# Optimization experiments

Measured on AMD Instinct MI355X. Metric: run time of the kernel, lower is better.

The kernel has to match this reference:

```python
import jax, jax.numpy as jnp
import numpy as np

ANGRES = 5  # u = v = angRes, n = 25


def _l2norm(x, axis):
    n = jnp.sqrt(jnp.sum(x * x, axis=axis, keepdims=True))
    return x / jnp.maximum(n, 1e-12)  # matches torch F.normalize eps


def _cos_attn(qm, km, vm):
    # qm: (b, M, K), km: (b, K, M), vm: (b, M, K)
    q = _l2norm(qm, -1)
    k = _l2norm(km, -2)
    att = jax.nn.softmax(q @ k, axis=-1)  # (b, M, M)
    return att @ vm


def _af_attn(x, u, v):  # AngularFrequencyAttention: b c (u v) h w -> b (c u) (h v w)
    b, c, n, h, w = x.shape
    t = x.reshape(b, c, u, v, h, w)
    qm = t.transpose(0, 1, 2, 4, 3, 5).reshape(b, c * u, h * v * w)   # (b,c,u,h,v,w)
    km = t.transpose(0, 4, 3, 5, 1, 2).reshape(b, h * v * w, c * u)   # (b,h,v,w,c,u)
    o = _cos_attn(qm, km, qm)
    o = o.reshape(b, c, u, h, v, w).transpose(0, 1, 2, 4, 3, 5).reshape(b, c, n, h, w)
    return o + x


def _sa_attn(x, u, v):  # SpatialAngularAttention: b c (u v) h w -> b (h u) (c v w)
    b, c, n, h, w = x.shape
    t = x.reshape(b, c, u, v, h, w)
    qm = t.transpose(0, 4, 2, 1, 3, 5).reshape(b, h * u, c * v * w)   # (b,h,u,c,v,w)
    km = t.transpose(0, 1, 3, 5, 4, 2).reshape(b, c * v * w, h * u)   # (b,c,v,w,h,u)
    o = _cos_attn(qm, km, qm)
    o = o.reshape(b, h, u, c, v, w).transpose(0, 3, 2, 4, 1, 5).reshape(b, c, n, h, w)
    return o + x


def _sf_attn(x, u, v):  # SpatialFrequencyAttention: b c (u v) h w -> b (c h) (w u v)
    b, c, n, h, w = x.shape
    t = x.reshape(b, c, u, v, h, w)
    qm = t.transpose(0, 1, 4, 5, 2, 3).reshape(b, c * h, w * u * v)   # (b,c,h,w,u,v)
    km = t.transpose(0, 5, 2, 3, 1, 4).reshape(b, w * u * v, c * h)   # (b,w,u,v,c,h)
    o = _cos_attn(qm, km, qm)
    o = o.reshape(b, c, h, w, u, v).transpose(0, 1, 4, 5, 2, 3).reshape(b, c, n, h, w)
    return o + x


def _layernorm(x, g, bta, eps=1e-5):
    mu = jnp.mean(x, -1, keepdims=True)
    var = jnp.mean(jnp.square(x - mu), -1, keepdims=True)
    return (x - mu) * jax.lax.rsqrt(var + eps) * g + bta


def setup_inputs() -> dict:
    key = jax.random.key(0)
    k0, k1, k2 = jax.random.split(key, 3)
    b, c, n, h, w = 4, 64, 25, 48, 48
    x = jax.random.normal(k0, (b, c, n, h, w), dtype=jnp.float32)
    gamma = jnp.ones((3 * c,), dtype=jnp.float32)
    beta = jnp.zeros((3 * c,), dtype=jnp.float32)
    w1 = jax.random.normal(k1, (3 * c, c), dtype=jnp.float32) * 0.02
    w2 = jax.random.normal(k2, (c, c), dtype=jnp.float32) * 0.02
    return {"x": x, "gamma": gamma, "beta": beta, "w1": w1, "w2": w2}


def reference(x, gamma, beta, w1, w2):
    u = v = ANGRES
    b, c, n, h, w = x.shape
    sf = _sf_attn(x, u, v)
    af = _af_attn(x, u, v)
    sa = _sa_attn(x, u, v)
    cat = jnp.concatenate([sf, af, sa], axis=1)            # (b, 3c, n, h, w)
    f = cat.transpose(0, 3, 4, 2, 1).reshape(b * h * w, n, 3 * c)
    y = _layernorm(f, gamma, beta)
    y = jax.nn.relu(y @ w1) @ w2                            # (bhw, n, c); dropout p=0.01 is eval-identity
    out = y.reshape(b, h, w, n, c).transpose(0, 4, 3, 1, 2) + x
    return out
```

## Files before the change

kernel.cpp:

```cpp
#include <hip/hip_runtime.h>
#include <stdint.h>

typedef __attribute__((ext_vector_type(8))) short bf16x8;
typedef __attribute__((ext_vector_type(4))) float f32x4;

__device__ __forceinline__ float b2f(short s) {
  union { unsigned u; float f; } a; a.u = ((unsigned)(unsigned short)s) << 16; return a.f;
}
__device__ __forceinline__ short f2b(float f) {
  union { float f; unsigned u; } a; a.f = f;
  unsigned r = a.u + 0x7fffu + ((a.u >> 16) & 1u);
  return (short)(r >> 16);
}
__device__ __forceinline__ void gload16(const void* g, void* l) {
  __builtin_amdgcn_global_load_lds((__attribute__((address_space(1))) void*)g,
                                   (__attribute__((address_space(3))) void*)l, 16, 0, 0);
}

#define SWZ(row, col) ((col) ^ (((row) & 7) << 3))

__global__ __launch_bounds__(256) void permute_sf_k(const float* __restrict__ x,
                                                    short* __restrict__ Q,
                                                    float* __restrict__ inv) {
  __shared__ float buf[4][1200];
  int wave = threadIdx.x >> 6, lane = threadIdx.x & 63;
  int gr = blockIdx.x * 4 + wave;
  int b = gr / 3072, m = gr - b * 3072;
  int c = m / 48, hh = m - c * 48;
  const float* xb = x + (long)(b * 64 + c) * 57600 + hh * 48;
  for (int uv = 0; uv < 25; ++uv)
    if (lane < 48) buf[wave][uv * 48 + lane] = xb[uv * 2304 + lane];
  __syncthreads();
  short* Qr = Q + (long)gr * 1280;
  float ss = 0.f;
  for (int k = lane; k < 1280; k += 64) {
    float v = 0.f;
    if (k < 1200) { int wv = k / 25, uv = k - wv * 25; v = buf[wave][uv * 48 + wv]; }
    ss += v * v;
    Qr[k] = f2b(v);
  }
  #pragma unroll
  for (int o = 32; o >= 1; o >>= 1) ss += __shfl_xor(ss, o, 64);
  if (lane == 0) inv[gr] = 1.0f / fmaxf(sqrtf(ss), 1e-12f);
}

__global__ __launch_bounds__(256) void permtr_all_k(const float* __restrict__ x,
    short* __restrict__ Qaf, short* __restrict__ QTaf,
    short* __restrict__ Qsa, short* __restrict__ QTsa,
    float* __restrict__ ssaf, float* __restrict__ sssa) {
  __shared__ short t[32][33];
  int bid = blockIdx.x;
  int isAF = (bid < 17280);
  int M, Mp, Kp, kt, mt, b;
  short *Q, *QT; float* ss;
  if (isAF) { M = 320; Mp = 384; Kp = 11520; kt = bid % 360; int r = bid / 360; mt = r % 12; b = r / 12;
              Q = Qaf; QT = QTaf; ss = ssaf; }
  else { int id = bid - 17280; M = 240; Mp = 256; Kp = 15360; kt = id % 480; int r = id / 480; mt = r % 8; b = r / 8;
         Q = Qsa; QT = QTsa; ss = sssa; }
  int k0 = kt * 32, m0 = mt * 32;
  int tx = threadIdx.x & 31, ty = threadIdx.x >> 5;
  const float* xb = x + (long)b * 3686400;
  #pragma unroll
  for (int i = 0; i < 32; i += 8) {
    int m = m0 + ty + i, k = k0 + tx;
    float v = 0.f;
    if (m < M) {
      int q1 = k / 240, r2 = k - q1 * 240;
      int v5 = r2 / 48, wv = r2 - v5 * 48;
      int a1 = m / 5, u = m - a1 * 5;
      long xi = isAF ? ((long)a1 * 25 + u * 5 + v5) * 2304 + q1 * 48 + wv
                     : ((long)q1 * 25 + u * 5 + v5) * 2304 + a1 * 48 + wv;
      v = xb[xi];
    }
    t[ty + i][tx] = f2b(v);
  }
  __syncthreads();
  long Qb = (long)b * Mp * Kp;
  #pragma unroll
  for (int i = 0; i < 32; i += 8)
    Q[Qb + (long)(m0 + ty + i) * Kp + k0 + tx] = t[ty + i][tx];
  #pragma unroll
  for (int i = 0; i < 32; i += 8)
    QT[Qb + (long)(k0 + ty + i) * Mp + m0 + tx] = t[tx][ty + i];
  if (threadIdx.x < 32 && m0 + (int)threadIdx.x < M) {
    float s = 0.f;
    #pragma unroll
    for (int k = 0; k < 32; ++k) { float f = b2f(t[threadIdx.x][k]); s += f * f; }
    atomicAdd(&ss[b * Mp + m0 + threadIdx.x], s);
  }
}

__global__ __launch_bounds__(256) void transpose_k(const short* __restrict__ in, short* __restrict__ out,
                                                   int R, int C) {
  __shared__ short t[32][33];
  long base = (long)blockIdx.z * R * C;
  int c0 = blockIdx.x * 32, r0 = blockIdx.y * 32;
  int tx = threadIdx.x & 31, ty = threadIdx.x >> 5;
  #pragma unroll
  for (int i = 0; i < 32; i += 8)
    t[ty + i][tx] = in[base + (long)(r0 + ty + i) * C + c0 + tx];
  __syncthreads();
  #pragma unroll
  for (int i = 0; i < 32; i += 8)
    out[base + (long)(c0 + ty + i) * R + r0 + tx] = t[tx][ty + i];
}

__global__ __launch_bounds__(256, 2) void gemm1_tri_k(const short* __restrict__ Q,
                                                      const float* __restrict__ invn,
                                                      short* __restrict__ att,
                                                      float* __restrict__ rowsum) {
  __shared__ short sm[32768];
  int tid = threadIdx.x, wave = tid >> 6, lane = tid & 63;
  int la = lane & 15, lb = lane >> 4;
  int bat = blockIdx.z;
  int bx = blockIdx.x, yt = 0, rem = bx;
  while (rem >= 24 - yt) { rem -= 24 - yt; ++yt; }
  int xt = yt + rem;
  const short* Qb = Q + (long)bat * 3932160L;
  const float* inv = invn + (long)bat * 3072;
  int row0 = yt * 128, col0 = xt * 128;
  f32x4 acc[4][4] = {};
  int wr = wave >> 1, wc = wave & 1;
  int rloc = tid >> 3, cbase = (tid & 7) * 8;
  int ldsoff = tid * 8;

  const short *pA[4], *pB[4];
  #pragma unroll
  for (int p = 0; p < 4; ++p) {
    int row = p * 32 + rloc;
    int sc = SWZ(row, cbase);
    pA[p] = Qb + (long)(row0 + row) * 1280 + sc;
    pB[p] = Qb + (long)(col0 + row) * 1280 + sc;
  }

  #define TRI_STAGE(KT, BUF) { \
    short* Asb = sm + (BUF) * 16384; \
    short* Bsb = Asb + 8192; \
    _Pragma("unroll") \
    for (int p = 0; p < 4; ++p) { \
      gload16(pA[p] + (KT) * 64, (void*)(Asb + p * 2048 + ldsoff)); \
      gload16(pB[p] + (KT) * 64, (void*)(Bsb + p * 2048 + ldsoff)); \
    } }
  #define TRI_COMP(BUF) { \
    const short* Asb = sm + (BUF) * 16384; \
    const short* Bsb = Asb + 8192; \
    _Pragma("unroll") \
    for (int kk = 0; kk < 64; kk += 32) { \
      bf16x8 av[4], bv[4]; \
      _Pragma("unroll") \
      for (int m = 0; m < 4; ++m) \
        av[m] = *(const bf16x8*)&Asb[(wr * 64 + m * 16 + la) * 64 + SWZ(la, kk + lb * 8)]; \
      _Pragma("unroll") \
      for (int nn = 0; nn < 4; ++nn) \
        bv[nn] = *(const bf16x8*)&Bsb[(wc * 64 + nn * 16 + la) * 64 + SWZ(la, kk + lb * 8)]; \
      _Pragma("unroll") \
      for (int m = 0; m < 4; ++m) \
        _Pragma("unroll") \
        for (int nn = 0; nn < 4; ++nn) \
          acc[m][nn] = __builtin_amdgcn_mfma_f32_16x16x32_bf16(av[m], bv[nn], acc[m][nn], 0, 0, 0); \
    } }

  TRI_STAGE(0, 0)
  for (int kt = 0; kt < 19; ++kt) {
    TRI_STAGE(kt + 1, (kt + 1) & 1)
    asm volatile("s_waitcnt vmcnt(8)" ::: "memory");
    __builtin_amdgcn_s_barrier();
    TRI_COMP(kt & 1)
    asm volatile("" ::: "memory");
    __builtin_amdgcn_s_barrier();
  }
  asm volatile("s_waitcnt vmcnt(0)" ::: "memory");
  __builtin_amdgcn_s_barrier();
  TRI_COMP(1)
  asm volatile("" ::: "memory");
  __builtin_amdgcn_s_barrier();

  short* staged = sm;
  #pragma unroll
  for (int m = 0; m < 4; ++m) {
    #pragma unroll
    for (int nn = 0; nn < 4; ++nn) {
      int cl = wc * 64 + nn * 16 + la;
      float ic = inv[col0 + cl];
      #pragma unroll
      for (int j = 0; j < 4; ++j) {
        int rl = wr * 64 + m * 16 + lb * 4 + j;
        staged[rl * 136 + cl] = f2b(__expf(acc[m][nn][j] * inv[row0 + rl] * ic));
      }
    }
  }
  __syncthreads();
  short* attb = att + (long)bat * 9437184L;
  float* rsb = rowsum + (long)bat * 3072;
  {
    int r = tid >> 1, half = tid & 1;
    short* dst = attb + (long)(row0 + r) * 3072 + col0 + half * 64;
    const short* src = &staged[r * 136 + half * 64];
    float s = 0.f;
    #pragma unroll
    for (int q = 0; q < 8; ++q) {
      bf16x8 v = *(const bf16x8*)&src[q * 8];
      *(bf16x8*)&dst[q * 8] = v;
      #pragma unroll
      for (int jj = 0; jj < 8; ++jj) s += b2f(v[jj]);
    }
    s += __shfl_xor(s, 1, 64);
    if (half == 0) atomicAdd(&rsb[row0 + r], s);
  }
  if (xt != yt) {
    int c = tid >> 1, half = tid & 1;
    short* dst = attb + (long)(col0 + c) * 3072 + row0 + half * 64;
    float s = 0.f;
    #pragma unroll
    for (int q = 0; q < 8; ++q) {
      bf16x8 o;
      #pragma unroll
      for (int jj = 0; jj < 8; ++jj) {
        o[jj] = staged[(half * 64 + q * 8 + jj) * 136 + c];
        s += b2f(o[jj]);
      }
      *(bf16x8*)&dst[q * 8] = o;
    }
    s += __shfl_xor(s, 1, 64);
    if (half == 0) atomicAdd(&rsb[col0 + c], s);
  }
}

__global__ __launch_bounds__(256, 2) void gemm_s_all_k(
    const short* __restrict__ Aaf, const short* __restrict__ Asa,
    float* __restrict__ Sfaf, float* __restrict__ Sfsa)
{
  __shared__ short sm[32768];
  int bid = blockIdx.x;
  const short* A; float* Sf;
  int lda, ktotal, ksper, ldc, row0, col0, bat, kc;
  long sA, sS;
  if (bid < 288) {
    int txy = bid % 9, z = bid / 9;
    col0 = (txy % 3) * 128; row0 = (txy / 3) * 128;
    bat = z / 8; kc = z % 8;
    lda = 11520; ktotal = 180; ksper = 23; ldc = 384;
    sA = 4423680L; sS = 147456L; A = Aaf; Sf = Sfaf;
  } else {
    int id = bid - 288;
    int txy = id % 4, z = id / 4;
    col0 = (txy % 2) * 128; row0 = (txy / 2) * 128;
    bat = z / 16; kc = z % 16;
    lda = 15360; ktotal = 240; ksper = 15; ldc = 256;
    sA = 3932160L; sS = 65536L; A = Asa; Sf = Sfsa;
  }
  int tid = threadIdx.x;
  int wave = tid >> 6, lane = tid & 63;
  int la = lane & 15, lb = lane >> 4;
  const short* Ab = A + (long)bat * sA;
  int kb = kc * ksper, ke = min(ktotal, kb + ksper);
  int L = ke - kb;
  f32x4 acc[4][4] = {};
  int wr = wave >> 1, wc = wave & 1;
  int rloc = tid >> 3, cbase = (tid & 7) * 8;
  int ldsoff = tid * 8;

  const short *pA[4], *pB[4];
  #pragma unroll
  for (int p = 0; p < 4; ++p) {
    int row = p * 32 + rloc;
    int sc = SWZ(row, cbase);
    pA[p] = Ab + (long)(row0 + row) * lda + sc;
    pB[p] = Ab + (long)(col0 + row) * lda + sc;
  }

  #define GS_STAGE(KT, BUF) { \
    short* Asb = sm + (BUF) * 16384; \
    short* Bsb = Asb + 8192; \
    _Pragma("unroll") \
    for (int p = 0; p < 4; ++p) { \
      gload16(pA[p] + (KT) * 64, (void*)(Asb + p * 2048 + ldsoff)); \
      gload16(pB[p] + (KT) * 64, (void*)(Bsb + p * 2048 + ldsoff)); \
    } }
  #define GS_COMP(BUF) { \
    const short* Asb = sm + (BUF) * 16384; \
    const short* Bsb = Asb + 8192; \
    _Pragma("unroll") \
    for (int kk = 0; kk < 64; kk += 32) { \
      bf16x8 av[4], bv[4]; \
      _Pragma("unroll") \
      for (int m = 0; m < 4; ++m) \
        av[m] = *(const bf16x8*)&Asb[(wr * 64 + m * 16 + la) * 64 + SWZ(la, kk + lb * 8)]; \
      _Pragma("unroll") \
      for (int nn = 0; nn < 4; ++nn) \
        bv[nn] = *(const bf16x8*)&Bsb[(wc * 64 + nn * 16 + la) * 64 + SWZ(la, kk + lb * 8)]; \
      _Pragma("unroll") \
      for (int m = 0; m < 4; ++m) \
        _Pragma("unroll") \
        for (int nn = 0; nn < 4; ++nn) \
          acc[m][nn] = __builtin_amdgcn_mfma_f32_16x16x32_bf16(av[m], bv[nn], acc[m][nn], 0, 0, 0); \
    } }

  GS_STAGE(kb, 0)
  for (int t = 0; t < L - 1; ++t) {
    GS_STAGE(kb + t + 1, (t + 1) & 1)
    asm volatile("s_waitcnt vmcnt(8)" ::: "memory");
    __builtin_amdgcn_s_barrier();
    GS_COMP(t & 1)
    asm volatile("" ::: "memory");
    __builtin_amdgcn_s_barrier();
  }
  asm volatile("s_waitcnt vmcnt(0)" ::: "memory");
  __builtin_amdgcn_s_barrier();
  GS_COMP((L - 1) & 1)

  float* Sb = Sf + (long)bat * sS;
  #pragma unroll
  for (int m = 0; m < 4; ++m) {
    int gr0 = row0 + wr * 64 + m * 16 + lb * 4;
    #pragma unroll
    for (int nn = 0; nn < 4; ++nn) {
      int gc = col0 + wc * 64 + nn * 16 + la;
      #pragma unroll
      for (int j = 0; j < 4; ++j)
        atomicAdd(&Sb[(long)(gr0 + j) * ldc + gc], acc[m][nn][j]);
    }
  }
}

__global__ __launch_bounds__(256) void softmax_all_k(
    const float* __restrict__ Sfaf, const float* __restrict__ Sfsa,
    const float* __restrict__ ssaf, const float* __restrict__ sssa,
    short* __restrict__ attaf, short* __restrict__ attsa)
{
  int wave = threadIdx.x >> 6, lane = threadIdx.x & 63;
  int rid = blockIdx.x * 4 + wave;
  int row, b, Mv, Mp; const float *Sf, *ss; short* att;
  if (rid < 1280) { row = rid % 320; b = rid / 320; Mv = 320; Mp = 384; Sf = Sfaf; ss = ssaf; att = attaf; }
  else { int id = rid - 1280; row = id % 240; b = id / 240; Mv = 240; Mp = 256; Sf = Sfsa; ss = sssa; att = attsa; }
  long sS = (long)Mp * Mp;
  const float* Sr = Sf + (long)b * sS + (long)row * Mp;
  const float* ssb = ss + b * Mp;
  float inv_i = rsqrtf(fmaxf(ssb[row], 1e-24f));
  float ev[6] = {0.f, 0.f, 0.f, 0.f, 0.f, 0.f};
  float sum = 0.f;
  #pragma unroll
  for (int q = 0; q < 6; ++q) {
    int j = q * 64 + lane;
    if (j < Mv) {
      float e = __expf(Sr[j] * inv_i * rsqrtf(fmaxf(ssb[j], 1e-24f)));
      ev[q] = e; sum += e;
    }
  }
  #pragma unroll
  for (int o = 32; o >= 1; o >>= 1) sum += __shfl_xor(sum, o, 64);
  float rden = 1.0f / sum;
  short* ar = att + (long)b * sS + (long)row * Mp;
  #pragma unroll
  for (int q = 0; q < 6; ++q) {
    int j = q * 64 + lane;
    if (j < Mp) ar[j] = (j < Mv) ? f2b(ev[q] * rden) : (short)0;
  }
}

__global__ __launch_bounds__(256, 2) void gemm2sf_k(const short* __restrict__ A,
                                                    const short* __restrict__ B,
                                                    const float* __restrict__ rowsum,
                                                    short* __restrict__ F) {
  __shared__ short sm[32768];
  int tid = threadIdx.x, wave = tid >> 6, lane = tid & 63;
  int la = lane & 15, lb = lane >> 4;
  int wr = wave >> 1, wc = wave & 1;
  int wk;
  { int xcd = blockIdx.x & 7, j = blockIdx.x >> 3; wk = xcd * 120 + j; }
  int yt = wk % 24, rem = wk / 24;
  int xt = rem % 10, bat = rem / 10;
  const short* Ab = A + (long)bat * 9437184L;
  const short* Bb = B + (long)bat * 3932160L;
  int rloc = tid >> 3, cbase = (tid & 7) * 8;
  int ldsoff = tid * 8;
  f32x4 acc[4][4] = {};

  const short *pA[4], *pB[4];
  #pragma unroll
  for (int p = 0; p < 4; ++p) {
    int row = p * 32 + rloc;
    int sc = SWZ(row, cbase);
    int rga = (row & 63) * 48 + yt * 2 + (row >> 6);
    pA[p] = Ab + (long)rga * 3072 + sc;
    int rgb = xt * 128 + row;
    pB[p] = Bb + (long)rgb * 3072 + sc;
  }

  #define G2_STAGE(KT, BUF) { \
    short* Asb = sm + (BUF) * 16384; \
    short* Bsb = Asb + 8192; \
    _Pragma("unroll") \
    for (int p = 0; p < 4; ++p) { \
      gload16(pA[p] + (KT) * 64, (void*)(Asb + p * 2048 + ldsoff)); \
      gload16(pB[p] + (KT) * 64, (void*)(Bsb + p * 2048 + ldsoff)); \
    } }
  #define G2_COMP(BUF) { \
    const short* Asb = sm + (BUF) * 16384; \
    const short* Bsb = Asb + 8192; \
    _Pragma("unroll") \
    for (int kk = 0; kk < 64; kk += 32) { \
      bf16x8 av[4], bv[4]; \
      _Pragma("unroll") \
      for (int m = 0; m < 4; ++m) \
        av[m] = *(const bf16x8*)&Asb[(wr * 64 + m * 16 + la) * 64 + SWZ(la, kk + lb * 8)]; \
      _Pragma("unroll") \
      for (int nn = 0; nn < 4; ++nn) \
        bv[nn] = *(const bf16x8*)&Bsb[(wc * 64 + nn * 16 + la) * 64 + SWZ(la, kk + lb * 8)]; \
      _Pragma("unroll") \
      for (int m = 0; m < 4; ++m) \
        _Pragma("unroll") \
        for (int nn = 0; nn < 4; ++nn) \
          acc[m][nn] = __builtin_amdgcn_mfma_f32_16x16x32_bf16(av[m], bv[nn], acc[m][nn], 0, 0, 0); \
    } }

  G2_STAGE(0, 0)
  for (int kt = 0; kt < 47; ++kt) {
    G2_STAGE(kt + 1, (kt + 1) & 1)
    asm volatile("s_waitcnt vmcnt(8)" ::: "memory");
    __builtin_amdgcn_s_barrier();
    G2_COMP(kt & 1)
    asm volatile("" ::: "memory");
    __builtin_amdgcn_s_barrier();
  }
  asm volatile("s_waitcnt vmcnt(0)" ::: "memory");
  __builtin_amdgcn_s_barrier();
  G2_COMP(1)
  asm volatile("" ::: "memory");
  __builtin_amdgcn_s_barrier();

  const float* rsb = rowsum + (long)bat * 3072;
  float rs[4][4];
  #pragma unroll
  for (int m = 0; m < 4; ++m)
    #pragma unroll
    for (int j = 0; j < 4; ++j)
      rs[m][j] = 1.0f / rsb[(m * 16 + lb * 4 + j) * 48 + yt * 2 + wr];

  short* staged = sm;
  #pragma unroll
  for (int m = 0; m < 4; ++m) {
    #pragma unroll
    for (int nn = 0; nn < 4; ++nn) {
      int cc = wc * 64 + nn * 16 + la;
      short4 o;
      o.x = f2b(acc[m][nn][0] * rs[m][0]); o.y = f2b(acc[m][nn][1] * rs[m][1]);
      o.z = f2b(acc[m][nn][2] * rs[m][2]); o.w = f2b(acc[m][nn][3] * rs[m][3]);
      *(short4*)&staged[(cc * 2 + wr) * 72 + m * 16 + lb * 4] = o;
    }
  }
  __syncthreads();
  #pragma unroll
  for (int rd = 0; rd < 8; ++rd) {
    int chunk = rd * 32 + (tid >> 3);
    int part = tid & 7;
    bf16x8 v = *(const bf16x8*)&staged[chunk * 72 + part * 8];
    int cc = chunk >> 1, sub = chunk & 1;
    int gc = xt * 128 + cc;
    if (gc < 1200) {
      int hh = yt * 2 + sub;
      int wv = gc / 25, nidx = gc - wv * 25;
      long base = (((long)(bat * 48 + hh) * 48 + wv) * 25 + nidx) * 192 + part * 8;
      *(bf16x8*)&F[base] = v;
    }
  }
}

__global__ __launch_bounds__(256) void gemm2_afsa_k(
    const short* __restrict__ attaf, const short* __restrict__ QTaf,
    const short* __restrict__ attsa, const short* __restrict__ QTsa,
    short* __restrict__ F)
{
  __shared__ short sm[20480];
  short* As = sm;
  short* Bs = sm + 4096;
  int bid = blockIdx.x;
  int isAF = (bid < 900);
  int NX, NY, LDA, KST, wk;
  const short *A, *B; long SA, SB;
  if (isAF) {
    NX = 45; NY = 5; LDA = 384; KST = 6; SA = 147456L; SB = 4423680L; A = attaf; B = QTaf;
    int xcd = bid & 7, j = bid >> 3;
    wk = (xcd < 4) ? xcd * 113 + j : 4 * 113 + (xcd - 4) * 112 + j;
  } else {
    NX = 60; NY = 4; LDA = 256; KST = 4; SA = 65536L; SB = 3932160L; A = attsa; B = QTsa;
    int id = bid - 900;
    int xcd = id & 7, j = id >> 3;
    wk = xcd * 120 + j;
  }
  int yt = wk % NY, rem = wk / NY;
  int xt = rem % NX, bat = rem / NX;
  int tid = threadIdx.x, wave = tid >> 6, lane = tid & 63;
  int la = lane & 15, lb = lane >> 4;
  const short* Ab = A + (long)bat * SA;
  const short* Bb = B + (long)bat * SB;
  f32x4 acc[4][4] = {};
  int rloc = tid >> 3, cbase = (tid & 7) * 8;
  int ldsoff = tid * 8;

  const short *pA[2], *pB[8];
  #pragma unroll
  for (int p = 0; p < 2; ++p) {
    int r = p * 32 + rloc;
    int sc = SWZ(r, cbase);
    int rowg = isAF ? (r * 5 + yt) : (yt * 64 + r);
    pA[p] = Ab + (long)rowg * LDA + sc;
  }
  #pragma unroll
  for (int p = 0; p < 8; ++p) {
    int rb = p * 32 + rloc;
    int sc = SWZ(rb, cbase);
    int rowg;
    if (isAF) rowg = xt * 256 + rb;
    else { int c = rb & 63, g = rb >> 6; rowg = c * 240 + xt * 4 + g; }
    pB[p] = Bb + (long)rowg * LDA + sc;
  }

  for (int kt = 0; kt < KST; ++kt) {
    #pragma unroll
    for (int p = 0; p < 2; ++p)
      gload16(pA[p] + kt * 64, (void*)(As + p * 2048 + ldsoff));
    #pragma unroll
    for (int p = 0; p < 8; ++p)
      gload16(pB[p] + kt * 64, (void*)(Bs + p * 2048 + ldsoff));
    __syncthreads();
    #pragma unroll
    for (int kk = 0; kk < 64; kk += 32) {
      bf16x8 av[4], bv[4];
      #pragma unroll
      for (int m = 0; m < 4; ++m)
        av[m] = *(const bf16x8*)&As[(m * 16 + la) * 64 + SWZ(la, kk + lb * 8)];
      #pragma unroll
      for (int nn = 0; nn < 4; ++nn)
        bv[nn] = *(const bf16x8*)&Bs[(wave * 64 + nn * 16 + la) * 64 + SWZ(la, kk + lb * 8)];
      #pragma unroll
      for (int m = 0; m < 4; ++m)
        #pragma unroll
        for (int nn = 0; nn < 4; ++nn)
          acc[m][nn] = __builtin_amdgcn_mfma_f32_16x16x32_bf16(av[m], bv[nn], acc[m][nn], 0, 0, 0);
    }
    __syncthreads();
  }

  short* staged = sm;
  #pragma unroll
  for (int m = 0; m < 4; ++m) {
    #pragma unroll
    for (int nn = 0; nn < 4; ++nn) {
      if (!isAF) {
        #pragma unroll
        for (int j = 0; j < 4; ++j)
          staged[((m * 16 + lb * 4 + j) * 4 + wave) * 72 + nn * 16 + la] = f2b(acc[m][nn][j]);
      } else {
        short4 o;
        o.x = f2b(acc[m][nn][0]); o.y = f2b(acc[m][nn][1]);
        o.z = f2b(acc[m][nn][2]); o.w = f2b(acc[m][nn][3]);
        *(short4*)&staged[(wave * 64 + nn * 16 + la) * 72 + m * 16 + lb * 4] = o;
      }
    }
  }
  __syncthreads();

  #pragma unroll
  for (int rd = 0; rd < 8; ++rd) {
    int chunk = rd * 32 + (tid >> 3);
    int part = tid & 7;
    bf16x8 v = *(const bf16x8*)&staged[chunk * 72 + part * 8];
    long base; bool ok = true;
    if (isAF) {
      int gc = xt * 256 + chunk;
      int hh = gc / 240, r2 = gc - hh * 240, v5 = r2 / 48, wv = r2 - v5 * 48;
      base = (((long)(bat * 48 + hh) * 48 + wv) * 25 + yt * 5 + v5) * 192 + 64 + part * 8;
    } else {
      int r = chunk >> 2, g = chunk & 3;
      int gr = yt * 64 + r; ok = (gr < 240);
      int hh = gr / 5, u = gr - hh * 5;
      int r2 = xt * 4 + g, v5 = r2 / 48, wv = r2 - v5 * 48;
      base = (((long)(bat * 48 + hh) * 48 + wv) * 25 + u * 5 + v5) * 192 + 128 + part * 8;
    }
    if (ok) *(bf16x8*)&F[base] = v;
  }
}

__global__ __launch_bounds__(256) void prep_w_k(const float* __restrict__ w1, const float* __restrict__ w2,
                                                short* __restrict__ w1t, short* __restrict__ w2t) {
  int idx = blockIdx.x * 256 + threadIdx.x;
  if (idx < 12288) {
    int i = idx / 64, j = idx - i * 64;
    w1t[j * 192 + i] = f2b(w1[idx]);
  } else if (idx < 16384) {
    int k = idx - 12288;
    int i = k / 64, j = k - i * 64;
    w2t[j * 64 + i] = f2b(w2[k]);
  }
}

__global__ __launch_bounds__(256) void ln_mlp_mfma_k(
    const short* __restrict__ F, const float* __restrict__ x,
    const float* __restrict__ gamma, const float* __restrict__ beta,
    const short* __restrict__ w1t, const short* __restrict__ w2t,
    float* __restrict__ out)
{
  int n = blockIdx.x, hh = blockIdx.y, b = blockIdx.z;
  __shared__ short A1[48 * 200];
  __shared__ float xs[64 * 49];
  __shared__ __align__(16) char pool[19584];
  short* Fs = (short*)pool;
  short* Y1 = (short*)pool;
  float* Y2 = (float*)(pool + 6912);
  int tid = threadIdx.x, wave = tid >> 6, lane = tid & 63;
  int la = lane & 15, lb = lane >> 4;
  long Fb0 = ((long)(b * 48 + hh) * 1200 + n) * 192;
  long xb = (long)b * 3686400 + (long)n * 2304 + hh * 48;

  #pragma unroll
  for (int it = 0; it < 5; ++it) {
    int ci = tid + 256 * it;
    if (ci < 1152) {
      int r = ci / 24, q = ci - r * 24;
      gload16(&F[Fb0 + (long)r * 4800 + q * 8], (void*)(Fs + ci * 8));
    }
  }
  {
    int ch = tid >> 2, qq = tid & 3;
    const float* xr = x + xb + (long)ch * 57600 + qq * 12;
    #pragma unroll
    for (int i = 0; i < 12; ++i) xs[ch * 49 + qq * 12 + i] = xr[i];
  }
  __syncthreads();

  float g0 = gamma[lane], g1 = gamma[lane + 64], g2 = gamma[lane + 128];
  float bt0 = beta[lane], bt1 = beta[lane + 64], bt2 = beta[lane + 128];
  #pragma unroll 4
  for (int rr = 0; rr < 12; ++rr) {
    int r = wave * 12 + rr;
    float xv = xs[lane * 49 + r];
    float v0 = b2f(Fs[r * 192 + lane]) + xv;
    float v1 = b2f(Fs[r * 192 + lane + 64]) + xv;
    float v2 = b2f(Fs[r * 192 + lane + 128]) + xv;
    float s = v0 + v1 + v2;
    #pragma unroll
    for (int o = 32; o >= 1; o >>= 1) s += __shfl_xor(s, o, 64);
    float mu = s * (1.f / 192.f);
    float d0 = v0 - mu, d1 = v1 - mu, d2 = v2 - mu;
    float q = d0 * d0 + d1 * d1 + d2 * d2;
    #pragma unroll
    for (int o = 32; o >= 1; o >>= 1) q += __shfl_xor(q, o, 64);
    float rs = rsqrtf(q * (1.f / 192.f) + 1e-5f);
    A1[r * 200 + lane]       = f2b(d0 * rs * g0 + bt0);
    A1[r * 200 + lane + 64]  = f2b(d1 * rs * g1 + bt1);
    A1[r * 200 + lane + 128] = f2b(d2 * rs * g2 + bt2);
  }
  __syncthreads();

  f32x4 acc1[3] = {};
  #pragma unroll
  for (int ks = 0; ks < 6; ++ks) {
    bf16x8 bv = *(const bf16x8*)&w1t[(wave * 16 + la) * 192 + ks * 32 + lb * 8];
    #pragma unroll
    for (int m = 0; m < 3; ++m) {
      bf16x8 av = *(const bf16x8*)&A1[(m * 16 + la) * 200 + ks * 32 + lb * 8];
      acc1[m] = __builtin_amdgcn_mfma_f32_16x16x32_bf16(av, bv, acc1[m], 0, 0, 0);
    }
  }
  #pragma unroll
  for (int m = 0; m < 3; ++m)
    #pragma unroll
    for (int j = 0; j < 4; ++j)
      Y1[(m * 16 + lb * 4 + j) * 72 + wave * 16 + la] = f2b(fmaxf(acc1[m][j], 0.f));
  __syncthreads();

  f32x4 acc2[3] = {};
  #pragma unroll
  for (int ks = 0; ks < 2; ++ks) {
    bf16x8 bv = *(const bf16x8*)&w2t[(wave * 16 + la) * 64 + ks * 32 + lb * 8];
    #pragma unroll
    for (int m = 0; m < 3; ++m) {
      bf16x8 av = *(const bf16x8*)&Y1[(m * 16 + la) * 72 + ks * 32 + lb * 8];
      acc2[m] = __builtin_amdgcn_mfma_f32_16x16x32_bf16(av, bv, acc2[m], 0, 0, 0);
    }
  }
  #pragma unroll
  for (int m = 0; m < 3; ++m)
    #pragma unroll
    for (int j = 0; j < 4; ++j)
      Y2[(m * 16 + lb * 4 + j) * 66 + wave * 16 + la] = acc2[m][j];
  __syncthreads();

  #pragma unroll
  for (int i = 0; i < 12; ++i) {
    int e = tid + 256 * i;
    int cc = e / 48, wv = e - cc * 48;
    out[xb + (long)cc * 57600 + wv] = Y2[wv * 66 + cc] + xs[cc * 49 + wv];
  }
}

extern "C" void kernel_launch(void* const* d_in, const int* in_sizes, int n_in,
                              void* d_out, int out_size, void* d_ws, size_t ws_size,
                              hipStream_t stream) {
  (void)in_sizes; (void)n_in; (void)out_size;
  const float* x     = (const float*)d_in[0];
  const float* gamma = (const float*)d_in[1];
  const float* beta  = (const float*)d_in[2];
  const float* w1    = (const float*)d_in[3];
  const float* w2    = (const float*)d_in[4];
  float* out = (float*)d_out;

  const size_t NEED = 237191168UL;
  if (ws_size < NEED) return;
  char* ws = (char*)d_ws;
  short* F     = (short*)(ws);
  short* attsf = (short*)(ws + 88473600UL);
  short* Qsf   = (short*)(ws + 163971072UL);
  short* QTsf  = (short*)(ws + 199360512UL);
  float* rowsum = (float*)(ws + 234749952UL);
  float* invn  = (float*)(ws + 237109248UL);
  short* w1t   = (short*)(ws + 237158400UL);
  short* w2t   = (short*)(ws + 237182976UL);
  short* Qaf   = (short*)(ws + 88473600UL);
  short* QTaf  = (short*)(ws + 123863040UL);
  float* Sfsa  = (float*)(ws + 159252480UL);
  float* ssaf  = (float*)(ws + 160301056UL);
  float* sssa  = (float*)(ws + 160307200UL);
  short* attaf = (short*)(ws + 160311296UL);
  short* attsa = (short*)(ws + 161490944UL);
  short* Qsa   = (short*)(ws + 163971072UL);
  short* QTsa  = (short*)(ws + 195428352UL);
  float* Sfaf  = (float*)(ws + 234749952UL);

  prep_w_k<<<64, 256, 0, stream>>>(w1, w2, w1t, w2t);

  permute_sf_k<<<3072, 256, 0, stream>>>(x, Qsf, invn);
  transpose_k<<<dim3(40, 96, 4), 256, 0, stream>>>(Qsf, QTsf, 3072, 1280);
  hipMemsetAsync(rowsum, 0, 49152, stream);
  gemm1_tri_k<<<dim3(300, 1, 4), 256, 0, stream>>>(Qsf, invn, attsf, rowsum);
  gemm2sf_k<<<dim3(960), 256, 0, stream>>>(attsf, QTsf, rowsum, F);

  hipMemsetAsync(Sfaf, 0, 2359296, stream);
  hipMemsetAsync(Sfsa, 0, 1048576, stream);
  hipMemsetAsync(ssaf, 0, 10240, stream);
  permtr_all_k<<<32640, 256, 0, stream>>>(x, Qaf, QTaf, Qsa, QTsa, ssaf, sssa);
  gemm_s_all_k<<<544, 256, 0, stream>>>(Qaf, Qsa, Sfaf, Sfsa);
  softmax_all_k<<<560, 256, 0, stream>>>(Sfaf, Sfsa, ssaf, sssa, attaf, attsa);
  gemm2_afsa_k<<<1860, 256, 0, stream>>>(attaf, QTaf, attsa, QTsa, F);

  ln_mlp_mfma_k<<<dim3(25, 48, 4), 256, 0, stream>>>(F, x, gamma, beta, w1t, w2t, out);
}
```

Before: 488.5 us.

## Enlarge SF gemm2 tile to 256x256 with 8 waves and phased prefetch

The SF attention-times-V GEMM moves from 128x128 tiles on 4 waves to 256x256 tiles on 8 waves (512 threads, 128KB LDS, 240 blocks). Each k-step is split into four compute phases, each interleaved with partial global-to-LDS prefetches and waitcnt barriers, and MFMA sections run with raised s_setprio. The goal is more data reuse per loaded byte and better overlap of loads with compute. The trade-offs are fewer blocks (240, against 960 before) and lower occupancy, which could leave compute units idle. The epilogue staging is also reworked with an XOR swizzle.

```diff
diff --git a/kernel.cpp b/kernel.cpp
--- a/kernel.cpp
+++ b/kernel.cpp
@@ -358,107 +358,127 @@
   }
 }
 
-__global__ __launch_bounds__(256, 2) void gemm2sf_k(const short* __restrict__ A,
-                                                    const short* __restrict__ B,
-                                                    const float* __restrict__ rowsum,
-                                                    short* __restrict__ F) {
-  __shared__ short sm[32768];
-  int tid = threadIdx.x, wave = tid >> 6, lane = tid & 63;
+__global__ __launch_bounds__(512) void gemm2sf_k(const short* __restrict__ A,
+                                                 const short* __restrict__ B,
+                                                 const float* __restrict__ rowsum,
+                                                 short* __restrict__ F) {
+  __shared__ short sm[65536];
+  int tid = threadIdx.x;
+  int wave = tid >> 6, lane = tid & 63;
   int la = lane & 15, lb = lane >> 4;
-  int wr = wave >> 1, wc = wave & 1;
+  int wr = wave >> 2, wc = wave & 3;
   int wk;
-  { int xcd = blockIdx.x & 7, j = blockIdx.x >> 3; wk = xcd * 120 + j; }
-  int yt = wk % 24, rem = wk / 24;
-  int xt = rem % 10, bat = rem / 10;
+  { int xcd = blockIdx.x & 7, j = blockIdx.x >> 3; wk = xcd * 30 + j; }
+  int yt = wk % 12, rem = wk / 12;
+  int xt = rem % 5, bat = rem / 5;
   const short* Ab = A + (long)bat * 9437184L;
   const short* Bb = B + (long)bat * 3932160L;
-  int rloc = tid >> 3, cbase = (tid & 7) * 8;
-  int ldsoff = tid * 8;
-  f32x4 acc[4][4] = {};
-
-  const short *pA[4], *pB[4];
-  #pragma unroll
-  for (int p = 0; p < 4; ++p) {
-    int row = p * 32 + rloc;
-    int sc = SWZ(row, cbase);
-    int rga = (row & 63) * 48 + yt * 2 + (row >> 6);
-    pA[p] = Ab + (long)rga * 3072 + sc;
-    int rgb = xt * 128 + row;
-    pB[p] = Bb + (long)rgb * 3072 + sc;
-  }
-
-  #define G2_STAGE(KT, BUF) { \
-    short* Asb = sm + (BUF) * 16384; \
-    short* Bsb = Asb + 8192; \
-    _Pragma("unroll") \
-    for (int p = 0; p < 4; ++p) { \
-      gload16(pA[p] + (KT) * 64, (void*)(Asb + p * 2048 + ldsoff)); \
-      gload16(pB[p] + (KT) * 64, (void*)(Bsb + p * 2048 + ldsoff)); \
-    } }
-  #define G2_COMP(BUF) { \
-    const short* Asb = sm + (BUF) * 16384; \
-    const short* Bsb = Asb + 8192; \
-    _Pragma("unroll") \
-    for (int kk = 0; kk < 64; kk += 32) { \
-      bf16x8 av[4], bv[4]; \
-      _Pragma("unroll") \
-      for (int m = 0; m < 4; ++m) \
-        av[m] = *(const bf16x8*)&Asb[(wr * 64 + m * 16 + la) * 64 + SWZ(la, kk + lb * 8)]; \
+  int rloc = tid >> 3;
+  int cbase = (tid & 7) * 8;
+  int sc = cbase ^ ((rloc & 7) << 3);
+  const short *pAg[4], *pBg[4];
+  #pragma unroll
+  for (int g = 0; g < 4; ++g) {
+    pAg[g] = Ab + (long)(rloc * 48 + yt * 4 + g) * 3072 + sc;
+    pBg[g] = Bb + (long)(xt * 256 + g * 64 + rloc) * 3072 + sc;
+  }
+  f32x4 acc[8][4] = {};
+
+  #pragma unroll
+  for (int g = 0; g < 4; ++g) {
+    gload16(pAg[g], (void*)(sm + g * 4096 + tid * 8));
+    gload16(pBg[g], (void*)(sm + 16384 + g * 4096 + tid * 8));
+  }
+  asm volatile("s_waitcnt vmcnt(0)" ::: "memory");
+  __builtin_amdgcn_s_barrier();
+
+  #define G2_PHASE(MH, KK, LOADB) { \
+    if (LOADB) { \
       _Pragma("unroll") \
       for (int nn = 0; nn < 4; ++nn) \
-        bv[nn] = *(const bf16x8*)&Bsb[(wc * 64 + nn * 16 + la) * 64 + SWZ(la, kk + lb * 8)]; \
+        bv[nn] = *(const bf16x8*)&Bsb[(wc * 64 + nn * 16 + la) * 64 + SWZ(la, (KK) + lb * 8)]; \
+    } \
+    _Pragma("unroll") \
+    for (int m = 0; m < 4; ++m) \
+      av[m] = *(const bf16x8*)&Asb[(wr * 128 + (MH) * 64 + m * 16 + la) * 64 + SWZ(la, (KK) + lb * 8)]; \
+    __builtin_amdgcn_s_setprio(1); \
+    _Pragma("unroll") \
+    for (int m = 0; m < 4; ++m) \
       _Pragma("unroll") \
-      for (int m = 0; m < 4; ++m) \
-        _Pragma("unroll") \
-        for (int nn = 0; nn < 4; ++nn) \
-          acc[m][nn] = __builtin_amdgcn_mfma_f32_16x16x32_bf16(av[m], bv[nn], acc[m][nn], 0, 0, 0); \
-    } }
-
-  G2_STAGE(0, 0)
-  for (int kt = 0; kt < 47; ++kt) {
-    G2_STAGE(kt + 1, (kt + 1) & 1)
-    asm volatile("s_waitcnt vmcnt(8)" ::: "memory");
+      for (int nn = 0; nn < 4; ++nn) \
+        acc[(MH) * 4 + m][nn] = __builtin_amdgcn_mfma_f32_16x16x32_bf16(av[m], bv[nn], acc[(MH) * 4 + m][nn], 0, 0, 0); \
+    __builtin_amdgcn_s_setprio(0); \
+  }
+
+  for (int t = 0; t < 48; ++t) {
+    const short* Asb = sm + (t & 1) * 32768;
+    const short* Bsb = Asb + 16384;
+    short* An = sm + ((t + 1) & 1) * 32768;
+    short* Bn = An + 16384;
+    int k1 = (t + 1) * 64;
+    bool pf = (t < 47);
+    bf16x8 av[4], bv[4];
+
+    asm volatile("s_waitcnt vmcnt(2)" ::: "memory");
     __builtin_amdgcn_s_barrier();
-    G2_COMP(kt & 1)
-    asm volatile("" ::: "memory");
+    if (pf) { gload16(pBg[0] + k1, (void*)(Bn + tid * 8));
+              gload16(pBg[1] + k1, (void*)(Bn + 4096 + tid * 8)); }
+    G2_PHASE(0, 0, 1)
+    asm volatile("s_waitcnt vmcnt(2)" ::: "memory");
     __builtin_amdgcn_s_barrier();
-  }
-  asm volatile("s_waitcnt vmcnt(0)" ::: "memory");
-  __builtin_amdgcn_s_barrier();
-  G2_COMP(1)
-  asm volatile("" ::: "memory");
-  __builtin_amdgcn_s_barrier();
+    if (pf) { gload16(pBg[2] + k1, (void*)(Bn + 8192 + tid * 8));
+              gload16(pBg[3] + k1, (void*)(Bn + 12288 + tid * 8)); }
+    G2_PHASE(1, 0, 0)
+    asm volatile("s_waitcnt vmcnt(4)" ::: "memory");
+    __builtin_amdgcn_s_barrier();
+    if (pf) { gload16(pAg[0] + k1, (void*)(An + tid * 8));
+              gload16(pAg[2] + k1, (void*)(An + 8192 + tid * 8)); }
+    G2_PHASE(0, 32, 1)
+    asm volatile("s_waitcnt vmcnt(6)" ::: "memory");
+    __builtin_amdgcn_s_barrier();
+    if (pf) { gload16(pAg[1] + k1, (void*)(An + 4096 + tid * 8));
+              gload16(pAg[3] + k1, (void*)(An + 12288 + tid * 8)); }
+    G2_PHASE(1, 32, 0)
+  }
+  __syncthreads();
 
   const float* rsb = rowsum + (long)bat * 3072;
-  float rs[4][4];
-  #pragma unroll
-  for (int m = 0; m < 4; ++m)
-    #pragma unroll
-    for (int j = 0; j < 4; ++j)
-      rs[m][j] = 1.0f / rsb[(m * 16 + lb * 4 + j) * 48 + yt * 2 + wr];
-
+  float rs[8][4];
+  #pragma unroll
+  for (int m = 0; m < 8; ++m) {
+    int sub = wr * 2 + (m >> 2);
+    #pragma unroll
+    for (int j = 0; j < 4; ++j) {
+      int cc = (m & 3) * 16 + lb * 4 + j;
+      rs[m][j] = 1.0f / rsb[cc * 48 + yt * 4 + sub];
+    }
+  }
   short* staged = sm;
   #pragma unroll
-  for (int m = 0; m < 4; ++m) {
+  for (int m = 0; m < 8; ++m) {
+    int sub = wr * 2 + (m >> 2);
     #pragma unroll
     for (int nn = 0; nn < 4; ++nn) {
-      int cc = wc * 64 + nn * 16 + la;
+      int gcl = wc * 64 + nn * 16 + la;
+      int chunk = gcl * 4 + sub;
+      int key = (gcl & 7) << 3;
       short4 o;
       o.x = f2b(acc[m][nn][0] * rs[m][0]); o.y = f2b(acc[m][nn][1] * rs[m][1]);
       o.z = f2b(acc[m][nn][2] * rs[m][2]); o.w = f2b(acc[m][nn][3] * rs[m][3]);
-      *(short4*)&staged[(cc * 2 + wr) * 72 + m * 16 + lb * 4] = o;
-    }
-  }
-  __syncthreads();
-  #pragma unroll
-  for (int rd = 0; rd < 8; ++rd) {
-    int chunk = rd * 32 + (tid >> 3);
+      *(short4*)&staged[chunk * 64 + (((m & 3) * 16 + lb * 4) ^ key)] = o;
+    }
+  }
+  __syncthreads();
+  #pragma unroll
+  for (int i = 0; i < 16; ++i) {
+    int chunk = i * 64 + (tid >> 3);
     int part = tid & 7;
-    bf16x8 v = *(const bf16x8*)&staged[chunk * 72 + part * 8];
-    int cc = chunk >> 1, sub = chunk & 1;
-    int gc = xt * 128 + cc;
+    int gcl = chunk >> 2, sub = chunk & 3;
+    int key = (gcl & 7) << 3;
+    bf16x8 v = *(const bf16x8*)&staged[chunk * 64 + ((part * 8) ^ key)];
+    int gc = xt * 256 + gcl;
     if (gc < 1200) {
-      int hh = yt * 2 + sub;
+      int hh = yt * 4 + sub;
       int wv = gc / 25, nidx = gc - wv * 25;
       long base = (((long)(bat * 48 + hh) * 48 + wv) * 25 + nidx) * 192 + part * 8;
       *(bf16x8*)&F[base] = v;
@@ -646,10 +666,10 @@
     float q = d0 * d0 + d1 * d1 + d2 * d2;
     #pragma unroll
     for (int o = 32; o >= 1; o >>= 1) q += __shfl_xor(q, o, 64);
-    float rs = rsqrtf(q * (1.f / 192.f) + 1e-5f);
-    A1[r * 200 + lane]       = f2b(d0 * rs * g0 + bt0);
-    A1[r * 200 + lane + 64]  = f2b(d1 * rs * g1 + bt1);
-    A1[r * 200 + lane + 128] = f2b(d2 * rs * g2 + bt2);
+    float rsq = rsqrtf(q * (1.f / 192.f) + 1e-5f);
+    A1[r * 200 + lane]       = f2b(d0 * rsq * g0 + bt0);
+    A1[r * 200 + lane + 64]  = f2b(d1 * rsq * g1 + bt1);
+    A1[r * 200 + lane + 128] = f2b(d2 * rsq * g2 + bt2);
   }
   __syncthreads();
 
@@ -734,7 +754,7 @@
   transpose_k<<<dim3(40, 96, 4), 256, 0, stream>>>(Qsf, QTsf, 3072, 1280);
   hipMemsetAsync(rowsum, 0, 49152, stream);
   gemm1_tri_k<<<dim3(300, 1, 4), 256, 0, stream>>>(Qsf, invn, attsf, rowsum);
-  gemm2sf_k<<<dim3(960), 256, 0, stream>>>(attsf, QTsf, rowsum, F);
+  gemm2sf_k<<<dim3(240), 512, 0, stream>>>(attsf, QTsf, rowsum, F);
 
   hipMemsetAsync(Sfaf, 0, 2359296, stream);
   hipMemsetAsync(Sfsa, 0, 1048576, stream);
```

Result: faster. 466.5 us (-4.5%).
